# Kernel optimization log

Measured on AMD Instinct MI355X. Metric: run time of the kernel, lower is better.

Reference implementation:

```python
import jax, jax.numpy as jnp
import numpy as np

IOU_THRESHOLD = 0.5
LOW_BG_IOU = 0.1      # below this -> ignored
IMG_SIZE = 1024.0


def _make_boxes(key, n):
    kxy, kwh = jax.random.split(key)
    xy = jax.random.uniform(kxy, (n, 2), dtype=jnp.float32, maxval=IMG_SIZE * 0.8)
    wh = jax.random.uniform(kwh, (n, 2), dtype=jnp.float32, minval=8.0, maxval=IMG_SIZE * 0.2)
    return jnp.concatenate([xy, xy + wh], axis=-1)  # valid x1<x2, y1<y2


def setup_inputs() -> dict:
    key = jax.random.key(0)
    k1, k2, k3 = jax.random.split(key, 3)
    proposals = _make_boxes(k1, 200000)          # [N,4]
    gt_boxes = _make_boxes(k2, 128)              # [G,4]
    gt_labels = jax.random.randint(k3, (128,), 1, 21, dtype=jnp.int64)  # [G]
    return {"proposals": proposals, "gt_boxes": gt_boxes, "gt_labels": gt_labels}


def get_iou(boxes1, boxes2):
    # boxes1: [G,4], boxes2: [N,4] -> iou [G,N]
    area1 = (boxes1[:, 2] - boxes1[:, 0]) * (boxes1[:, 3] - boxes1[:, 1])  # [G]
    area2 = (boxes2[:, 2] - boxes2[:, 0]) * (boxes2[:, 3] - boxes2[:, 1])  # [N]
    x1 = jnp.maximum(boxes1[:, None, 0], boxes2[None, :, 0])
    y1 = jnp.maximum(boxes1[:, None, 1], boxes2[None, :, 1])
    x2 = jnp.minimum(boxes1[:, None, 2], boxes2[None, :, 2])
    y2 = jnp.minimum(boxes1[:, None, 3], boxes2[None, :, 3])
    inter = jnp.clip(x2 - x1, 0.0) * jnp.clip(y2 - y1, 0.0)  # [G,N]
    union = area1[:, None] + area2[None, :] - inter
    return inter / union


def reference(proposals, gt_boxes, gt_labels):
    iou = get_iou(gt_boxes, proposals)                # [G,N]
    best_match_iou = jnp.max(iou, axis=0)             # [N]
    best_match_gt_idx = jnp.argmax(iou, axis=0)       # [N], >= 0
    background = (best_match_iou < IOU_THRESHOLD) & (best_match_iou >= LOW_BG_IOU)
    ignored = best_match_iou < LOW_BG_IOU
    # torch clamps the (-1/-2) sentinel indices back to 0 before the gather,
    # so gathering with the raw argmax index is identical.
    matched_gt_boxes = gt_boxes[best_match_gt_idx]    # [N,4]
    labels = gt_labels[best_match_gt_idx].astype(jnp.int64)
    labels = jnp.where(background, jnp.int64(0), labels)
    labels = jnp.where(ignored, jnp.int64(-1), labels)
    return labels, matched_gt_boxes
```

## Files before the change

### kernel.cpp

```cpp
#include <hip/hip_runtime.h>


#define IOU_THRESHOLD 0.5f
#define LOW_BG_IOU 0.1f
#define BLOCK 256
#define PROPS 256

struct Cand { float i, u; int g; };

__device__ __forceinline__ Cand merge_up(Cand a, Cand b) {
    float p1 = b.i * a.u;
    float e1 = fmaf(b.i, a.u, -p1);
    float p2 = a.i * b.u;
    float e2 = fmaf(a.i, b.u, -p2);
    bool gt = (p1 - p2) > (e2 - e1);
    Cand r;
    r.i = gt ? b.i : a.i;
    r.u = gt ? b.u : a.u;
    r.g = gt ? b.g : a.g;
    return r;
}

__global__ __launch_bounds__(BLOCK) void roi_match_kernel(
    const float* __restrict__ proposals,
    const float* __restrict__ gt_boxes,
    const int*   __restrict__ gt_labels,
    float* __restrict__ out,
    int N)
{
#pragma clang fp contract(off)
    __shared__ float4 s_gt[128];
    __shared__ float  s_lab[128];
    __shared__ float4 s_part[2][PROPS];

    const int tid  = threadIdx.x;
    const int wave = tid >> 6;
    const int lane = tid & 63;
    const int h    = wave & 1;
    const int qt   = wave >> 1;
    const int base = blockIdx.x * PROPS;

    if (tid < 128) {
        s_gt[tid]  = ((const float4*)gt_boxes)[tid];
        s_lab[tid] = (float)gt_labels[tid];
    }
    __syncthreads();

    const int slot0 = h * 128 + lane;
    const int slot1 = slot0 + 64;
    const int n0 = base + slot0;
    const int n1 = base + slot1;
    const int c0 = n0 < N ? n0 : N - 1;
    const int c1 = n1 < N ? n1 : N - 1;
    const float4 P0 = ((const float4*)proposals)[c0];
    const float4 P1 = ((const float4*)proposals)[c1];
    const float a0 = (P0.z - P0.x) * (P0.w - P0.y);
    const float a1 = (P1.z - P1.x) * (P1.w - P1.y);

    const int gbase = qt * 64;
    Cand best0 = {0.0f, 1.0f, gbase};
    Cand best1 = {0.0f, 1.0f, gbase};

#pragma unroll 2
    for (int grp = 0; grp < 8; ++grp) {
        const int g0 = gbase + grp * 8;
        float4 gb[8];
        float  ga[8];
#pragma unroll
        for (int k = 0; k < 8; ++k) gb[k] = s_gt[g0 + k];
#pragma unroll
        for (int k = 0; k < 8; ++k)
            ga[k] = (gb[k].z - gb[k].x) * (gb[k].w - gb[k].y);

        {
            float iv[8], uv[8];
#pragma unroll
            for (int k = 0; k < 8; ++k) {
                float x1 = fmaxf(gb[k].x, P0.x);
                float y1 = fmaxf(gb[k].y, P0.y);
                float x2 = fminf(gb[k].z, P0.z);
                float y2 = fminf(gb[k].w, P0.w);
                float iw = fmaxf(x2 - x1, 0.0f);
                float ih = fmaxf(y2 - y1, 0.0f);
                iv[k] = iw * ih;
                uv[k] = (ga[k] + a0) - iv[k];
            }
            Cand c01 = merge_up(Cand{iv[0], uv[0], g0 + 0}, Cand{iv[1], uv[1], g0 + 1});
            Cand c23 = merge_up(Cand{iv[2], uv[2], g0 + 2}, Cand{iv[3], uv[3], g0 + 3});
            Cand c45 = merge_up(Cand{iv[4], uv[4], g0 + 4}, Cand{iv[5], uv[5], g0 + 5});
            Cand c67 = merge_up(Cand{iv[6], uv[6], g0 + 6}, Cand{iv[7], uv[7], g0 + 7});
            Cand c03 = merge_up(c01, c23);
            Cand c47 = merge_up(c45, c67);
            best0 = merge_up(best0, merge_up(c03, c47));
        }
        {
            float iv[8], uv[8];
#pragma unroll
            for (int k = 0; k < 8; ++k) {
                float x1 = fmaxf(gb[k].x, P1.x);
                float y1 = fmaxf(gb[k].y, P1.y);
                float x2 = fminf(gb[k].z, P1.z);
                float y2 = fminf(gb[k].w, P1.w);
                float iw = fmaxf(x2 - x1, 0.0f);
                float ih = fmaxf(y2 - y1, 0.0f);
                iv[k] = iw * ih;
                uv[k] = (ga[k] + a1) - iv[k];
            }
            Cand c01 = merge_up(Cand{iv[0], uv[0], g0 + 0}, Cand{iv[1], uv[1], g0 + 1});
            Cand c23 = merge_up(Cand{iv[2], uv[2], g0 + 2}, Cand{iv[3], uv[3], g0 + 3});
            Cand c45 = merge_up(Cand{iv[4], uv[4], g0 + 4}, Cand{iv[5], uv[5], g0 + 5});
            Cand c67 = merge_up(Cand{iv[6], uv[6], g0 + 6}, Cand{iv[7], uv[7], g0 + 7});
            Cand c03 = merge_up(c01, c23);
            Cand c47 = merge_up(c45, c67);
            best1 = merge_up(best1, merge_up(c03, c47));
        }
    }

    s_part[qt][slot0] = make_float4(best0.i, best0.u, __int_as_float(best0.g), 0.0f);
    s_part[qt][slot1] = make_float4(best1.i, best1.u, __int_as_float(best1.g), 0.0f);
    __syncthreads();

    const int n = base + tid;
    if (n < N) {
        float4 v0 = s_part[0][tid];
        float4 v1 = s_part[1][tid];
        Cand lo = {v0.x, v0.y, __float_as_int(v0.z)};
        Cand hi = {v1.x, v1.y, __float_as_int(v1.z)};
        Cand best = merge_up(lo, hi);

        float iou = best.i / best.u;

        float lab;
        if (iou < LOW_BG_IOU)          lab = -1.0f;
        else if (iou < IOU_THRESHOLD)  lab = 0.0f;
        else                           lab = s_lab[best.g];

        out[n] = lab;
        ((float4*)(out + N))[n] = s_gt[best.g];
    }
}

extern "C" void kernel_launch(void* const* d_in, const int* in_sizes, int n_in,
                              void* d_out, int out_size, void* d_ws, size_t ws_size,
                              hipStream_t stream) {
    const float* proposals = (const float*)d_in[0];
    const float* gt_boxes  = (const float*)d_in[1];
    const int*   gt_labels = (const int*)d_in[2];
    float* out = (float*)d_out;

    int N = in_sizes[0] / 4;
    int blocks = (N + PROPS - 1) / PROPS;

    roi_match_kernel<<<blocks, BLOCK, 0, stream>>>(proposals, gt_boxes,
                                                   gt_labels, out, N);
}
```

Baseline: 78.65 us.

## Split GT boxes four ways per block, one proposal per thread, precompute GT areas

```diff
diff --git a/kernel.cpp b/kernel.cpp
--- a/kernel.cpp
+++ b/kernel.cpp
@@ -4,7 +4,7 @@
 #define IOU_THRESHOLD 0.5f
 #define LOW_BG_IOU 0.1f
 #define BLOCK 256
-#define PROPS 256
+#define NPROP 64
 
 struct Cand { float i, u; int g; };
 
@@ -30,113 +30,96 @@
 {
 #pragma clang fp contract(off)
     __shared__ float4 s_gt[128];
+    __shared__ float  s_area[128];
     __shared__ float  s_lab[128];
-    __shared__ float4 s_part[2][PROPS];
+    __shared__ float4 s_part[4][NPROP];
 
     const int tid  = threadIdx.x;
     const int wave = tid >> 6;
     const int lane = tid & 63;
-    const int h    = wave & 1;
-    const int qt   = wave >> 1;
-    const int base = blockIdx.x * PROPS;
+    const int base = blockIdx.x * NPROP;
 
     if (tid < 128) {
-        s_gt[tid]  = ((const float4*)gt_boxes)[tid];
-        s_lab[tid] = (float)gt_labels[tid];
+        float4 b = ((const float4*)gt_boxes)[tid];
+        s_gt[tid]   = b;
+        s_area[tid] = (b.z - b.x) * (b.w - b.y);
+        s_lab[tid]  = (float)gt_labels[tid];
     }
     __syncthreads();
 
-    const int slot0 = h * 128 + lane;
-    const int slot1 = slot0 + 64;
-    const int n0 = base + slot0;
-    const int n1 = base + slot1;
-    const int c0 = n0 < N ? n0 : N - 1;
-    const int c1 = n1 < N ? n1 : N - 1;
-    const float4 P0 = ((const float4*)proposals)[c0];
-    const float4 P1 = ((const float4*)proposals)[c1];
-    const float a0 = (P0.z - P0.x) * (P0.w - P0.y);
-    const float a1 = (P1.z - P1.x) * (P1.w - P1.y);
+    const int n  = base + lane;
+    const int nc = n < N ? n : N - 1;
+    const float4 P = ((const float4*)proposals)[nc];
+    const float area_p = (P.z - P.x) * (P.w - P.y);
 
-    const int gbase = qt * 64;
-    Cand best0 = {0.0f, 1.0f, gbase};
-    Cand best1 = {0.0f, 1.0f, gbase};
+    const int gbase = wave * 32;
+    Cand best = {0.0f, 1.0f, gbase};
 
 #pragma unroll 2
     for (int grp = 0; grp < 8; ++grp) {
-        const int g0 = gbase + grp * 8;
-        float4 gb[8];
-        float  ga[8];
-#pragma unroll
-        for (int k = 0; k < 8; ++k) gb[k] = s_gt[g0 + k];
-#pragma unroll
-        for (int k = 0; k < 8; ++k)
-            ga[k] = (gb[k].z - gb[k].x) * (gb[k].w - gb[k].y);
+        const int g0 = gbase + grp * 4;
 
+        float4 gb0 = s_gt[g0 + 0];
+        float4 gb1 = s_gt[g0 + 1];
+        float4 gb2 = s_gt[g0 + 2];
+        float4 gb3 = s_gt[g0 + 3];
+        float ar0 = s_area[g0 + 0];
+        float ar1 = s_area[g0 + 1];
+        float ar2 = s_area[g0 + 2];
+        float ar3 = s_area[g0 + 3];
+
+        float iv[4], uv[4];
         {
-            float iv[8], uv[8];
-#pragma unroll
-            for (int k = 0; k < 8; ++k) {
-                float x1 = fmaxf(gb[k].x, P0.x);
-                float y1 = fmaxf(gb[k].y, P0.y);
-                float x2 = fminf(gb[k].z, P0.z);
-                float y2 = fminf(gb[k].w, P0.w);
-                float iw = fmaxf(x2 - x1, 0.0f);
-                float ih = fmaxf(y2 - y1, 0.0f);
-                iv[k] = iw * ih;
-                uv[k] = (ga[k] + a0) - iv[k];
-            }
-            Cand c01 = merge_up(Cand{iv[0], uv[0], g0 + 0}, Cand{iv[1], uv[1], g0 + 1});
-            Cand c23 = merge_up(Cand{iv[2], uv[2], g0 + 2}, Cand{iv[3], uv[3], g0 + 3});
-            Cand c45 = merge_up(Cand{iv[4], uv[4], g0 + 4}, Cand{iv[5], uv[5], g0 + 5});
-            Cand c67 = merge_up(Cand{iv[6], uv[6], g0 + 6}, Cand{iv[7], uv[7], g0 + 7});
-            Cand c03 = merge_up(c01, c23);
-            Cand c47 = merge_up(c45, c67);
-            best0 = merge_up(best0, merge_up(c03, c47));
+            float x1 = fmaxf(gb0.x, P.x), y1 = fmaxf(gb0.y, P.y);
+            float x2 = fminf(gb0.z, P.z), y2 = fminf(gb0.w, P.w);
+            float iw = fmaxf(x2 - x1, 0.0f), ih = fmaxf(y2 - y1, 0.0f);
+            iv[0] = iw * ih; uv[0] = (ar0 + area_p) - iv[0];
         }
         {
-            float iv[8], uv[8];
-#pragma unroll
-            for (int k = 0; k < 8; ++k) {
-                float x1 = fmaxf(gb[k].x, P1.x);
-                float y1 = fmaxf(gb[k].y, P1.y);
-                float x2 = fminf(gb[k].z, P1.z);
-                float y2 = fminf(gb[k].w, P1.w);
-                float iw = fmaxf(x2 - x1, 0.0f);
-                float ih = fmaxf(y2 - y1, 0.0f);
-                iv[k] = iw * ih;
-                uv[k] = (ga[k] + a1) - iv[k];
-            }
-            Cand c01 = merge_up(Cand{iv[0], uv[0], g0 + 0}, Cand{iv[1], uv[1], g0 + 1});
-            Cand c23 = merge_up(Cand{iv[2], uv[2], g0 + 2}, Cand{iv[3], uv[3], g0 + 3});
-            Cand c45 = merge_up(Cand{iv[4], uv[4], g0 + 4}, Cand{iv[5], uv[5], g0 + 5});
-            Cand c67 = merge_up(Cand{iv[6], uv[6], g0 + 6}, Cand{iv[7], uv[7], g0 + 7});
-            Cand c03 = merge_up(c01, c23);
-            Cand c47 = merge_up(c45, c67);
-            best1 = merge_up(best1, merge_up(c03, c47));
+            float x1 = fmaxf(gb1.x, P.x), y1 = fmaxf(gb1.y, P.y);
+            float x2 = fminf(gb1.z, P.z), y2 = fminf(gb1.w, P.w);
+            float iw = fmaxf(x2 - x1, 0.0f), ih = fmaxf(y2 - y1, 0.0f);
+            iv[1] = iw * ih; uv[1] = (ar1 + area_p) - iv[1];
         }
+        {
+            float x1 = fmaxf(gb2.x, P.x), y1 = fmaxf(gb2.y, P.y);
+            float x2 = fminf(gb2.z, P.z), y2 = fminf(gb2.w, P.w);
+            float iw = fmaxf(x2 - x1, 0.0f), ih = fmaxf(y2 - y1, 0.0f);
+            iv[2] = iw * ih; uv[2] = (ar2 + area_p) - iv[2];
+        }
+        {
+            float x1 = fmaxf(gb3.x, P.x), y1 = fmaxf(gb3.y, P.y);
+            float x2 = fminf(gb3.z, P.z), y2 = fminf(gb3.w, P.w);
+            float iw = fmaxf(x2 - x1, 0.0f), ih = fmaxf(y2 - y1, 0.0f);
+            iv[3] = iw * ih; uv[3] = (ar3 + area_p) - iv[3];
+        }
+
+        Cand c01 = merge_up(Cand{iv[0], uv[0], g0 + 0}, Cand{iv[1], uv[1], g0 + 1});
+        Cand c23 = merge_up(Cand{iv[2], uv[2], g0 + 2}, Cand{iv[3], uv[3], g0 + 3});
+        Cand c   = merge_up(c01, c23);
+        best = merge_up(best, c);
     }
 
-    s_part[qt][slot0] = make_float4(best0.i, best0.u, __int_as_float(best0.g), 0.0f);
-    s_part[qt][slot1] = make_float4(best1.i, best1.u, __int_as_float(best1.g), 0.0f);
+    s_part[wave][lane] = make_float4(best.i, best.u, __int_as_float(best.g), 0.0f);
     __syncthreads();
 
-    const int n = base + tid;
-    if (n < N) {
-        float4 v0 = s_part[0][tid];
-        float4 v1 = s_part[1][tid];
-        Cand lo = {v0.x, v0.y, __float_as_int(v0.z)};
-        Cand hi = {v1.x, v1.y, __float_as_int(v1.z)};
-        Cand best = merge_up(lo, hi);
-
-        float iou = best.i / best.u;
+    if (wave == 0 && n < N) {
+        float4 v0 = s_part[0][lane];
+        Cand b = {v0.x, v0.y, __float_as_int(v0.z)};
+#pragma unroll
+        for (int q = 1; q < 4; ++q) {
+            float4 v = s_part[q][lane];
+            b = merge_up(b, Cand{v.x, v.y, __float_as_int(v.z)});
+        }
+        float iou = b.i / b.u;
 
         float lab;
         if (iou < LOW_BG_IOU)          lab = -1.0f;
         else if (iou < IOU_THRESHOLD)  lab = 0.0f;
-        else                           lab = s_lab[best.g];
+        else                           lab = s_lab[b.g];
 
         out[n] = lab;
-        ((float4*)(out + N))[n] = s_gt[best.g];
+        ((float4*)(out + N))[n] = s_gt[b.g];
     }
 }
 
@@ -149,7 +132,7 @@
     float* out = (float*)d_out;
 
     int N = in_sizes[0] / 4;
-    int blocks = (N + PROPS - 1) / PROPS;
+    int blocks = (N + NPROP - 1) / NPROP;
 
     roi_match_kernel<<<blocks, BLOCK, 0, stream>>>(proposals, gt_boxes,
                                                    gt_labels, out, N);
```

Result: faster. 74.63 us (-5.1%).
